# Optimization experiments

Measured on AMD Instinct MI355X. Metric: run time of the kernel, lower is better.

## Reference

```python
import jax, jax.numpy as jnp
import numpy as np

T, B, E, H = 4096, 1, 256, 8
D = E // H  # head_dim = 32


def setup_inputs() -> dict:
    root = jax.random.key(0)
    ks = jax.random.split(root, 12)
    s = 0.02
    return {
        "query": jax.random.normal(ks[0], (T, B, E), dtype=jnp.float32),
        "key": jax.random.normal(ks[1], (T, B, E), dtype=jnp.float32),
        "value": jax.random.normal(ks[2], (T, B, E), dtype=jnp.float32),
        "residual_attn": jax.random.normal(ks[3], (H, T, T), dtype=jnp.float32),
        "Wq": jax.random.normal(ks[4], (E, E), dtype=jnp.float32) * s,
        "bq": jnp.zeros((E,), dtype=jnp.float32),
        "Wk": jax.random.normal(ks[5], (E, E), dtype=jnp.float32) * s,
        "bk": jnp.zeros((E,), dtype=jnp.float32),
        "Wv": jax.random.normal(ks[6], (E, E), dtype=jnp.float32) * s,
        "bv": jnp.zeros((E,), dtype=jnp.float32),
        "Wo": jax.random.normal(ks[7], (E, E), dtype=jnp.float32) * s,
        "bo": jnp.zeros((E,), dtype=jnp.float32),
    }


def reference(query, key, value, residual_attn, Wq, bq, Wk, bk, Wv, bv, Wo, bo):
    t, b, e = query.shape
    h = H
    d = e // h
    scaling = d ** (-0.5)
    # Original forward: `query = key = self.with_pos_embed(query, pos)` with pos=None,
    # so both q and k are projected from `query`; the `key` arg is ignored.
    qk_src = query
    q = (qk_src @ Wq.T + bq) * scaling          # [T, B, E]
    k = qk_src @ Wk.T + bk                       # [T, B, E]
    v = value @ Wv.T + bv                        # [T, B, E]

    def split_heads(x):
        # [T, B, E] -> [B, H, T, D]
        return x.reshape(t, b, h, d).transpose(1, 2, 0, 3)

    qh, kh, vh = split_heads(q), split_heads(k), split_heads(v)
    # scores: [B, H, T, S] with residual attention added pre-softmax
    scores = jnp.einsum('bhtd,bhsd->bhts', qh, kh) + residual_attn[None]
    attn = jax.nn.softmax(scores, axis=-1)       # dropout p=0.0 -> no-op
    out = jnp.einsum('bhts,bhsd->bhtd', attn, vh)  # [B, H, T, D]
    out = out.transpose(2, 0, 1, 3).reshape(t, b, e)  # [T, B, E]
    return out @ Wo.T + bo
```

## Files before the change

### kernel.cpp

```cpp
#include <hip/hip_runtime.h>
#include <hip/hip_bf16.h>

#define T_DIM 4096
#define E_DIM 256
#define H_DIM 8
#define D_DIM 32
#define SSPLIT 2

typedef __attribute__((ext_vector_type(8))) short short8;
typedef __attribute__((ext_vector_type(4))) float f32x4;

__device__ __forceinline__ unsigned short f2bf(float f) {
    union { float f; unsigned u; } x; x.f = f;
    return (unsigned short)((x.u + 0x7FFFu + ((x.u >> 16) & 1u)) >> 16);
}

struct CastArgs {
    const float* src[6];
    unsigned short* dst[6];
    int n4[6];
};

__global__ __launch_bounds__(256) void cast_kernel(CastArgs a) {
    int b = blockIdx.y;
    const float* s = a.src[b];
    unsigned short* d = a.dst[b];
    int n4 = a.n4[b];
    int i = blockIdx.x * 256 + threadIdx.x;
    if (i < n4) {
        float4 v = reinterpret_cast<const float4*>(s)[i];
        ushort4 o;
        o.x = f2bf(v.x); o.y = f2bf(v.y); o.z = f2bf(v.z); o.w = f2bf(v.w);
        reinterpret_cast<ushort4*>(d)[i] = o;
    }
}

__global__ __launch_bounds__(256) void proj_kernel(
    const unsigned short* __restrict__ qb, const unsigned short* __restrict__ vb,
    const unsigned short* __restrict__ wq, const unsigned short* __restrict__ wk,
    const unsigned short* __restrict__ wv,
    const float* __restrict__ bq, const float* __restrict__ bk, const float* __restrict__ bv,
    unsigned short* __restrict__ qw, unsigned short* __restrict__ kw,
    unsigned short* __restrict__ vt)
{
    const int z = blockIdx.z;
    const unsigned short* A = (z == 2) ? vb : qb;
    const unsigned short* W = (z == 0) ? wq : (z == 1) ? wk : wv;
    const float* bias = (z == 0) ? bq : (z == 1) ? bk : bv;

    const int tid = threadIdx.x;
    const int w = tid >> 6, lane = tid & 63;
    const int g = lane >> 4, r = lane & 15;
    const int t0 = blockIdx.x * 64 + w * 16;
    const int e0 = blockIdx.y * 64;

    f32x4 acc[4];
    const f32x4 zero = {0.f, 0.f, 0.f, 0.f};
    for (int i = 0; i < 4; i++) acc[i] = zero;

    for (int k0 = 0; k0 < E_DIM; k0 += 32) {
        short8 af = *(const short8*)(A + (size_t)(t0 + r) * E_DIM + k0 + g * 8);
        for (int et = 0; et < 4; et++) {
            short8 bf = *(const short8*)(W + (size_t)(e0 + et * 16 + r) * E_DIM + k0 + g * 8);
            acc[et] = __builtin_amdgcn_mfma_f32_16x16x32_bf16(af, bf, acc[et], 0, 0, 0);
        }
    }

    if (z < 2) {
        const float scale = (z == 0) ? 0.17677669529663687f : 1.0f;
        unsigned short* out = (z == 0) ? qw : kw;
        for (int et = 0; et < 4; et++) {
            int e = e0 + et * 16 + r;
            float b = bias[e];
            for (int j = 0; j < 4; j++) {
                int t = t0 + g * 4 + j;
                out[(size_t)t * E_DIM + e] = f2bf((acc[et][j] + b) * scale);
            }
        }
    } else {
        for (int et = 0; et < 4; et++) {
            int e = e0 + et * 16 + r;
            float b = bias[e];
            ushort4 pk;
            pk.x = f2bf(acc[et][0] + b);
            pk.y = f2bf(acc[et][1] + b);
            pk.z = f2bf(acc[et][2] + b);
            pk.w = f2bf(acc[et][3] + b);
            *(ushort4*)(vt + (size_t)e * T_DIM + t0 + g * 4) = pk;
        }
    }
}

__global__ __launch_bounds__(256) void flash_kernel(
    const unsigned short* __restrict__ qw, const unsigned short* __restrict__ kw,
    const unsigned short* __restrict__ vt, const float* __restrict__ residual,
    float* __restrict__ po, float* __restrict__ pl)
{
    __shared__ __align__(16) unsigned short plds[4][16][72];

    const int tid = threadIdx.x;
    const int w = tid >> 6, lane = tid & 63;
    const int g = lane >> 4, r = lane & 15;
    const int h = blockIdx.y;
    const int q0 = blockIdx.x * 64 + w * 16;
    const int sbeg = blockIdx.z * (T_DIM / SSPLIT);
    const int send = sbeg + (T_DIM / SSPLIT);

    short8 qf = *(const short8*)(qw + (size_t)(q0 + r) * E_DIM + h * D_DIM + g * 8);

    const f32x4 zero = {0.f, 0.f, 0.f, 0.f};
    f32x4 oacc[2]; oacc[0] = zero; oacc[1] = zero;
    float lacc[4] = {0.f, 0.f, 0.f, 0.f};

    const float* resbase = residual + (size_t)h * T_DIM * T_DIM;

    for (int s0 = sbeg; s0 < send; s0 += 64) {
        float res[4][4];
        for (int st = 0; st < 4; st++)
            for (int j = 0; j < 4; j++)
                res[st][j] = resbase[(size_t)(q0 + g * 4 + j) * T_DIM + s0 + st * 16 + r];

        short8 kf[4];
        for (int st = 0; st < 4; st++)
            kf[st] = *(const short8*)(kw + (size_t)(s0 + st * 16 + r) * E_DIM + h * D_DIM + g * 8);

        short8 vf[2][2];
        for (int dh = 0; dh < 2; dh++)
            for (int sf = 0; sf < 2; sf++)
                vf[dh][sf] = *(const short8*)(vt + (size_t)(h * D_DIM + dh * 16 + r) * T_DIM
                                              + s0 + sf * 32 + g * 8);

        for (int st = 0; st < 4; st++) {
            f32x4 s = __builtin_amdgcn_mfma_f32_16x16x32_bf16(qf, kf[st], zero, 0, 0, 0);
            for (int j = 0; j < 4; j++) {
                float p = __expf(s[j] + res[st][j]);
                lacc[j] += p;
                plds[w][g * 4 + j][st * 16 + r] = f2bf(p);
            }
        }

        short8 pa0 = *(const short8*)(&plds[w][r][g * 8]);
        short8 pa1 = *(const short8*)(&plds[w][r][32 + g * 8]);

        for (int dh = 0; dh < 2; dh++) {
            oacc[dh] = __builtin_amdgcn_mfma_f32_16x16x32_bf16(pa0, vf[dh][0], oacc[dh], 0, 0, 0);
            oacc[dh] = __builtin_amdgcn_mfma_f32_16x16x32_bf16(pa1, vf[dh][1], oacc[dh], 0, 0, 0);
        }
    }

    for (int j = 0; j < 4; j++) {
        float v = lacc[j];
        v += __shfl_xor(v, 1);
        v += __shfl_xor(v, 2);
        v += __shfl_xor(v, 4);
        v += __shfl_xor(v, 8);
        lacc[j] = v;
    }

    float* pob = po + ((size_t)blockIdx.z * H_DIM + h) * T_DIM * D_DIM;
    for (int dh = 0; dh < 2; dh++)
        for (int j = 0; j < 4; j++)
            pob[(size_t)(q0 + g * 4 + j) * D_DIM + dh * 16 + r] = oacc[dh][j];

    if (r == 0) {
        float* plb = pl + ((size_t)blockIdx.z * H_DIM + h) * T_DIM;
        for (int j = 0; j < 4; j++) plb[q0 + g * 4 + j] = lacc[j];
    }
}

__global__ __launch_bounds__(256) void combine_kernel(
    const float* __restrict__ po, const float* __restrict__ pl,
    unsigned short* __restrict__ attn)
{
    int idx = blockIdx.x * 256 + threadIdx.x;
    int idx4 = idx * 4;
    int t = idx4 / E_DIM;
    int e = idx4 % E_DIM;
    int h = e >> 5, d = e & 31;

    const size_t chunk = (size_t)H_DIM * T_DIM * D_DIM;
    const float* p0 = po + ((size_t)h * T_DIM + t) * D_DIM + d;
    float l = pl[(size_t)h * T_DIM + t] + pl[(size_t)(H_DIM + h) * T_DIM + t];
    float rl = 1.0f / l;

    float4 a = *(const float4*)p0;
    float4 b = *(const float4*)(p0 + chunk);
    ushort4 o;
    o.x = f2bf((a.x + b.x) * rl);
    o.y = f2bf((a.y + b.y) * rl);
    o.z = f2bf((a.z + b.z) * rl);
    o.w = f2bf((a.w + b.w) * rl);
    *(ushort4*)(attn + (size_t)t * E_DIM + e) = o;
}

__global__ __launch_bounds__(256) void oproj_kernel(
    const unsigned short* __restrict__ attn, const unsigned short* __restrict__ wo,
    const float* __restrict__ bo, float* __restrict__ out)
{
    const int tid = threadIdx.x;
    const int w = tid >> 6, lane = tid & 63;
    const int g = lane >> 4, r = lane & 15;
    const int t0 = blockIdx.x * 64 + w * 16;
    const int e0 = blockIdx.y * 64;

    f32x4 acc[4];
    const f32x4 zero = {0.f, 0.f, 0.f, 0.f};
    for (int i = 0; i < 4; i++) acc[i] = zero;

    for (int k0 = 0; k0 < E_DIM; k0 += 32) {
        short8 af = *(const short8*)(attn + (size_t)(t0 + r) * E_DIM + k0 + g * 8);
        for (int et = 0; et < 4; et++) {
            short8 bf = *(const short8*)(wo + (size_t)(e0 + et * 16 + r) * E_DIM + k0 + g * 8);
            acc[et] = __builtin_amdgcn_mfma_f32_16x16x32_bf16(af, bf, acc[et], 0, 0, 0);
        }
    }

    for (int et = 0; et < 4; et++) {
        int e = e0 + et * 16 + r;
        float b = bo[e];
        for (int j = 0; j < 4; j++) {
            int t = t0 + g * 4 + j;
            out[(size_t)t * E_DIM + e] = acc[et][j] + b;
        }
    }
}

extern "C" void kernel_launch(void* const* d_in, const int* in_sizes, int n_in,
                              void* d_out, int out_size, void* d_ws, size_t ws_size,
                              hipStream_t stream)
{
    const float* query    = (const float*)d_in[0];
    const float* value    = (const float*)d_in[2];
    const float* residual = (const float*)d_in[3];
    const float* Wq = (const float*)d_in[4];
    const float* bq = (const float*)d_in[5];
    const float* Wk = (const float*)d_in[6];
    const float* bk = (const float*)d_in[7];
    const float* Wv = (const float*)d_in[8];
    const float* bv = (const float*)d_in[9];
    const float* Wo = (const float*)d_in[10];
    const float* bo = (const float*)d_in[11];
    float* out = (float*)d_out;

    char* ws = (char*)d_ws;
    size_t off = 0;
    auto alloc = [&](size_t bytes) -> char* {
        char* p = ws + off;
        off = (off + bytes + 255) & ~(size_t)255;
        return p;
    };
    const size_t TE = (size_t)T_DIM * E_DIM;
    const size_t EE = (size_t)E_DIM * E_DIM;

    unsigned short* qb  = (unsigned short*)alloc(TE * 2);
    unsigned short* vb  = (unsigned short*)alloc(TE * 2);
    unsigned short* wqc = (unsigned short*)alloc(EE * 2);
    unsigned short* wkc = (unsigned short*)alloc(EE * 2);
    unsigned short* wvc = (unsigned short*)alloc(EE * 2);
    unsigned short* woc = (unsigned short*)alloc(EE * 2);
    unsigned short* qwp = (unsigned short*)alloc(TE * 2);
    unsigned short* kwp = (unsigned short*)alloc(TE * 2);
    unsigned short* vtp = (unsigned short*)alloc(TE * 2);
    unsigned short* attn = (unsigned short*)alloc(TE * 2);
    float* po = (float*)alloc((size_t)SSPLIT * H_DIM * T_DIM * D_DIM * 4);
    float* pl = (float*)alloc((size_t)SSPLIT * H_DIM * T_DIM * 4);

    CastArgs ca;
    ca.src[0] = query; ca.dst[0] = qb;  ca.n4[0] = (int)(TE / 4);
    ca.src[1] = value; ca.dst[1] = vb;  ca.n4[1] = (int)(TE / 4);
    ca.src[2] = Wq;    ca.dst[2] = wqc; ca.n4[2] = (int)(EE / 4);
    ca.src[3] = Wk;    ca.dst[3] = wkc; ca.n4[3] = (int)(EE / 4);
    ca.src[4] = Wv;    ca.dst[4] = wvc; ca.n4[4] = (int)(EE / 4);
    ca.src[5] = Wo;    ca.dst[5] = woc; ca.n4[5] = (int)(EE / 4);

    dim3 cgrid((unsigned)((TE / 4 + 255) / 256), 6);
    hipLaunchKernelGGL(cast_kernel, cgrid, dim3(256), 0, stream, ca);

    proj_kernel<<<dim3(T_DIM / 64, E_DIM / 64, 3), 256, 0, stream>>>(
        qb, vb, wqc, wkc, wvc, bq, bk, bv, qwp, kwp, vtp);

    flash_kernel<<<dim3(T_DIM / 64, H_DIM, SSPLIT), 256, 0, stream>>>(
        qwp, kwp, vtp, residual, po, pl);

    combine_kernel<<<dim3((unsigned)(TE / 4 / 256)), 256, 0, stream>>>(po, pl, attn);

    oproj_kernel<<<dim3(T_DIM / 64, E_DIM / 64), 256, 0, stream>>>(attn, woc, bo, out);
}
```

Baseline: 794.9 us.

## Transpose MFMA operands for vectorized residual loads and prefetch next tile

Swaps the A/B operands of both MFMAs so each lane owns one query row and four consecutive key columns. That lets the residual matrix be read with float4 loads, P be written to LDS as ushort4, and outputs be stored as float4. The residual tile for the next iteration is prefetched into registers, the per-row sum reduction becomes two shuffles, and launch bounds ask for four blocks per SIMD. The goal is better coalescing on the dominant residual stream and hiding its latency, at the cost of higher register pressure.

```diff
diff --git a/kernel.cpp b/kernel.cpp
--- a/kernel.cpp
+++ b/kernel.cpp
@@ -91,7 +91,7 @@
     }
 }
 
-__global__ __launch_bounds__(256) void flash_kernel(
+__global__ __launch_bounds__(256, 4) void flash_kernel(
     const unsigned short* __restrict__ qw, const unsigned short* __restrict__ kw,
     const unsigned short* __restrict__ vt, const float* __restrict__ residual,
     float* __restrict__ po, float* __restrict__ pl)
@@ -104,68 +104,77 @@
     const int h = blockIdx.y;
     const int q0 = blockIdx.x * 64 + w * 16;
     const int sbeg = blockIdx.z * (T_DIM / SSPLIT);
-    const int send = sbeg + (T_DIM / SSPLIT);
+    const int NT = (T_DIM / SSPLIT) / 64;
 
     short8 qf = *(const short8*)(qw + (size_t)(q0 + r) * E_DIM + h * D_DIM + g * 8);
 
     const f32x4 zero = {0.f, 0.f, 0.f, 0.f};
     f32x4 oacc[2]; oacc[0] = zero; oacc[1] = zero;
-    float lacc[4] = {0.f, 0.f, 0.f, 0.f};
-
-    const float* resbase = residual + (size_t)h * T_DIM * T_DIM;
-
-    for (int s0 = sbeg; s0 < send; s0 += 64) {
-        float res[4][4];
+    float lsum = 0.f;
+
+    const float* resptr = residual + (size_t)h * T_DIM * T_DIM
+                        + (size_t)(q0 + r) * T_DIM + sbeg + g * 4;
+    const unsigned short* kptr = kw + (size_t)(sbeg + r) * E_DIM + h * D_DIM + g * 8;
+    const unsigned short* vptr = vt + (size_t)(h * D_DIM + r) * T_DIM + sbeg + g * 8;
+
+    float4 resn[4];
+    #pragma unroll
+    for (int st = 0; st < 4; st++) resn[st] = *(const float4*)(resptr + st * 16);
+
+    for (int t = 0; t < NT; t++) {
+        float4 res[4];
+        #pragma unroll
+        for (int st = 0; st < 4; st++) res[st] = resn[st];
+        if (t + 1 < NT) {
+            const float* rp = resptr + (size_t)(t + 1) * 64;
+            #pragma unroll
+            for (int st = 0; st < 4; st++) resn[st] = *(const float4*)(rp + st * 16);
+        }
+
+        short8 kf[4];
+        #pragma unroll
         for (int st = 0; st < 4; st++)
-            for (int j = 0; j < 4; j++)
-                res[st][j] = resbase[(size_t)(q0 + g * 4 + j) * T_DIM + s0 + st * 16 + r];
-
-        short8 kf[4];
-        for (int st = 0; st < 4; st++)
-            kf[st] = *(const short8*)(kw + (size_t)(s0 + st * 16 + r) * E_DIM + h * D_DIM + g * 8);
-
+            kf[st] = *(const short8*)(kptr + (size_t)(t * 64 + st * 16) * E_DIM);
         short8 vf[2][2];
+        #pragma unroll
         for (int dh = 0; dh < 2; dh++)
+            #pragma unroll
             for (int sf = 0; sf < 2; sf++)
-                vf[dh][sf] = *(const short8*)(vt + (size_t)(h * D_DIM + dh * 16 + r) * T_DIM
-                                              + s0 + sf * 32 + g * 8);
-
+                vf[dh][sf] = *(const short8*)(vptr + (size_t)dh * 16 * T_DIM + t * 64 + sf * 32);
+
+        #pragma unroll
         for (int st = 0; st < 4; st++) {
-            f32x4 s = __builtin_amdgcn_mfma_f32_16x16x32_bf16(qf, kf[st], zero, 0, 0, 0);
-            for (int j = 0; j < 4; j++) {
-                float p = __expf(s[j] + res[st][j]);
-                lacc[j] += p;
-                plds[w][g * 4 + j][st * 16 + r] = f2bf(p);
-            }
+            f32x4 sT = __builtin_amdgcn_mfma_f32_16x16x32_bf16(kf[st], qf, zero, 0, 0, 0);
+            float p0 = __expf(sT[0] + res[st].x); lsum += p0;
+            float p1 = __expf(sT[1] + res[st].y); lsum += p1;
+            float p2 = __expf(sT[2] + res[st].z); lsum += p2;
+            float p3 = __expf(sT[3] + res[st].w); lsum += p3;
+            ushort4 pk;
+            pk.x = f2bf(p0); pk.y = f2bf(p1); pk.z = f2bf(p2); pk.w = f2bf(p3);
+            *(ushort4*)(&plds[w][r][st * 16 + g * 4]) = pk;
         }
 
         short8 pa0 = *(const short8*)(&plds[w][r][g * 8]);
         short8 pa1 = *(const short8*)(&plds[w][r][32 + g * 8]);
 
-        for (int dh = 0; dh < 2; dh++) {
-            oacc[dh] = __builtin_amdgcn_mfma_f32_16x16x32_bf16(pa0, vf[dh][0], oacc[dh], 0, 0, 0);
-            oacc[dh] = __builtin_amdgcn_mfma_f32_16x16x32_bf16(pa1, vf[dh][1], oacc[dh], 0, 0, 0);
-        }
-    }
-
-    for (int j = 0; j < 4; j++) {
-        float v = lacc[j];
-        v += __shfl_xor(v, 1);
-        v += __shfl_xor(v, 2);
-        v += __shfl_xor(v, 4);
-        v += __shfl_xor(v, 8);
-        lacc[j] = v;
-    }
+        oacc[0] = __builtin_amdgcn_mfma_f32_16x16x32_bf16(vf[0][0], pa0, oacc[0], 0, 0, 0);
+        oacc[0] = __builtin_amdgcn_mfma_f32_16x16x32_bf16(vf[0][1], pa1, oacc[0], 0, 0, 0);
+        oacc[1] = __builtin_amdgcn_mfma_f32_16x16x32_bf16(vf[1][0], pa0, oacc[1], 0, 0, 0);
+        oacc[1] = __builtin_amdgcn_mfma_f32_16x16x32_bf16(vf[1][1], pa1, oacc[1], 0, 0, 0);
+    }
+
+    lsum += __shfl_xor(lsum, 16);
+    lsum += __shfl_xor(lsum, 32);
 
     float* pob = po + ((size_t)blockIdx.z * H_DIM + h) * T_DIM * D_DIM;
-    for (int dh = 0; dh < 2; dh++)
-        for (int j = 0; j < 4; j++)
-            pob[(size_t)(q0 + g * 4 + j) * D_DIM + dh * 16 + r] = oacc[dh][j];
-
-    if (r == 0) {
-        float* plb = pl + ((size_t)blockIdx.z * H_DIM + h) * T_DIM;
-        for (int j = 0; j < 4; j++) plb[q0 + g * 4 + j] = lacc[j];
-    }
+    #pragma unroll
+    for (int dh = 0; dh < 2; dh++) {
+        float4 ov;
+        ov.x = oacc[dh][0]; ov.y = oacc[dh][1]; ov.z = oacc[dh][2]; ov.w = oacc[dh][3];
+        *(float4*)(pob + (size_t)(q0 + r) * D_DIM + dh * 16 + g * 4) = ov;
+    }
+    if (g == 0)
+        pl[((size_t)blockIdx.z * H_DIM + h) * T_DIM + q0 + r] = lsum;
 }
 
 __global__ __launch_bounds__(256) void combine_kernel(
```

Measured after the change: 814.5 us. 1.02x slower.
